# Optimization experiments

Measured on AMD Instinct MI355X. Metric: run time of the kernel, lower is better.

The kernel has to match this reference:

```python
import jax, jax.numpy as jnp
import numpy as np

B, T, I, H, O = 8192, 128, 28, 200, 10


def setup_inputs() -> dict:
    key = jax.random.key(0)
    ks = jax.random.split(key, 7)
    s_ih = 1.0 / np.sqrt(H)
    return {
        "x": jax.random.normal(ks[0], (B, T, I), dtype=jnp.float32),
        "W_ih": jax.random.uniform(ks[1], (H, I), jnp.float32, -s_ih, s_ih),
        "W_hh": jax.random.uniform(ks[2], (H, H), jnp.float32, -s_ih, s_ih),
        "b_ih": jax.random.uniform(ks[3], (H,), jnp.float32, -s_ih, s_ih),
        "b_hh": jax.random.uniform(ks[4], (H,), jnp.float32, -s_ih, s_ih),
        "W_fc": jax.random.uniform(ks[5], (O, H), jnp.float32, -s_ih, s_ih),
        "b_fc": jax.random.uniform(ks[6], (O,), jnp.float32, -s_ih, s_ih),
    }


def reference(x, W_ih, W_hh, b_ih, b_hh, W_fc, b_fc):
    # Precompute input projections for all timesteps in one GEMM: [B,T,H]
    xp = jnp.einsum("bti,hi->bth", x, W_ih) + b_ih + b_hh
    h0 = jnp.zeros((x.shape[0], W_hh.shape[0]), dtype=x.dtype)

    def step(h, xp_t):
        # h_t = relu(x_t W_ih^T + b_ih + h_{t-1} W_hh^T + b_hh)
        h = jax.nn.relu(xp_t + h @ W_hh.T)
        return h, None

    # scan over time: xp transposed to [T,B,H]
    h_last, _ = jax.lax.scan(step, h0, jnp.swapaxes(xp, 0, 1))
    # out[:, -1, :] then fc1
    return h_last @ W_fc.T + b_fc
```

## Files before the change

### kernel.cpp

```cpp
#include <hip/hip_runtime.h>

typedef float  f4v __attribute__((ext_vector_type(4)));
typedef float  f2v __attribute__((ext_vector_type(2)));
typedef short  s8v __attribute__((ext_vector_type(8)));

#define TT  128
#define II  28
#define HH  200
#define BB  16
#define NT  256
#define SH  264
#define KHX 208
#define SF  212

__device__ __forceinline__ short f2bf(float f) {
    union { float f; unsigned u; } a; a.f = f;
    unsigned r = a.u + 0x7FFFu + ((a.u >> 16) & 1u);
    return (short)(r >> 16);
}

__global__ __launch_bounds__(NT, 2)
void rnn_mfma(const float* __restrict__ x,
              const float* __restrict__ W_ih,
              const float* __restrict__ W_hh,
              const float* __restrict__ b_ih,
              const float* __restrict__ b_hh,
              const float* __restrict__ W_fc,
              const float* __restrict__ b_fc,
              float* __restrict__ out)
{
    __shared__ short Hs[BB][SH];
    __shared__ float Hf[BB][SF];
    __shared__ float bsum[208];

    const int tid  = threadIdx.x;
    const int lane = tid & 63;
    const int q    = lane >> 4;
    const int lr   = lane & 15;
    const int wave = tid >> 6;
    const int b0   = blockIdx.x * BB;

    const int first = (wave == 0) ? 0 : 1 + 3 * wave;
    const int cnt   = (wave == 0) ? 4 : 3;

    for (int i = tid; i < BB * SH / 2; i += NT) ((int*)Hs)[i] = 0;
    for (int j = tid; j < 208; j += NT) bsum[j] = (j < HH) ? b_ih[j] + b_hh[j] : 0.0f;

    s8v Af[4][8];
    #pragma unroll
    for (int u = 0; u < 4; ++u) {
        const int j = 16 * (first + u) + lr;
        #pragma unroll
        for (int kc = 0; kc < 8; ++kc) {
            const int k0 = 32 * kc + 8 * q;
            union { short s[8]; s8v v; } tv;
            #pragma unroll
            for (int i = 0; i < 8; ++i) {
                const int k = k0 + i;
                float w = 0.0f;
                if (u < cnt && j < HH) {
                    if (k < HH)                      w = W_hh[j * HH + k];
                    else if (k >= KHX && k < KHX+II) w = W_ih[j * II + (k - KHX)];
                }
                tv.s[i] = f2bf(w);
            }
            Af[u][kc] = tv.v;
        }
    }
    __syncthreads();

    f4v biasv[4];
    #pragma unroll
    for (int u = 0; u < 4; ++u) {
        const int jt = first + ((u < cnt) ? u : 0);
        biasv[u] = *(const f4v*)&bsum[16 * jt + 4 * q];
    }

    const int xr = tid / 14, xc = 2 * (tid % 14);
    f2v xcur = {0.f, 0.f}, xnxt = {0.f, 0.f};
    if (tid < 224) {
        f2v v0 = __builtin_nontemporal_load((const f2v*)&x[((b0 + xr) * TT + 0) * II + xc]);
        *(int*)&Hs[xr][KHX + xc] = (f2bf(v0.x) & 0xffff) | (f2bf(v0.y) << 16);
        xcur = __builtin_nontemporal_load((const f2v*)&x[((b0 + xr) * TT + 1) * II + xc]);
    }
    __syncthreads();

    for (int t = 0; t < TT; ++t) {
        if (tid < 224) {
            const int tn = (t + 2 < TT) ? t + 2 : TT - 1;
            xnxt = __builtin_nontemporal_load((const f2v*)&x[((b0 + xr) * TT + tn) * II + xc]);
        }

        f4v acc[4];
        #pragma unroll
        for (int u = 0; u < 4; ++u) acc[u] = biasv[u];

        #pragma unroll
        for (int kc = 0; kc < 8; ++kc) {
            const s8v bf = *(const s8v*)&Hs[lr][32 * kc + 8 * q];
            #pragma unroll
            for (int u = 0; u < 4; ++u)
                if (u < cnt)
                    acc[u] = __builtin_amdgcn_mfma_f32_16x16x32_bf16(Af[u][kc], bf, acc[u], 0, 0, 0);
        }
        __syncthreads();

        #pragma unroll
        for (int u = 0; u < 4; ++u) {
            if (u < cnt) {
                const int jt = first + u;
                const f4v a = acc[u];
                const float r0 = fmaxf(a.x, 0.f), r1 = fmaxf(a.y, 0.f);
                const float r2 = fmaxf(a.z, 0.f), r3 = fmaxf(a.w, 0.f);
                short4 hv;
                hv.x = f2bf(r0); hv.y = f2bf(r1); hv.z = f2bf(r2); hv.w = f2bf(r3);
                *(short4*)&Hs[lr][16 * jt + 4 * q] = hv;
                if (t == TT - 1) {
                    f4v rf = {r0, r1, r2, r3};
                    *(f4v*)&Hf[lr][16 * jt + 4 * q] = rf;
                }
            }
        }
        if (t < TT - 1 && tid < 224)
            *(int*)&Hs[xr][KHX + xc] = (f2bf(xcur.x) & 0xffff) | (f2bf(xcur.y) << 16);
        xcur = xnxt;
        __syncthreads();
    }

    if (tid < BB * 10) {
        const int o = tid >> 4, r = tid & 15;
        float s = b_fc[o];
        for (int k = 0; k < HH; ++k)
            s = fmaf(Hf[r][k], W_fc[o * HH + k], s);
        __builtin_nontemporal_store(s, &out[(b0 + r) * 10 + o]);
    }
}

extern "C" void kernel_launch(void* const* d_in, const int* in_sizes, int n_in,
                              void* d_out, int out_size, void* d_ws, size_t ws_size,
                              hipStream_t stream) {
    const float* x    = (const float*)d_in[0];
    const float* W_ih = (const float*)d_in[1];
    const float* W_hh = (const float*)d_in[2];
    const float* b_ih = (const float*)d_in[3];
    const float* b_hh = (const float*)d_in[4];
    const float* W_fc = (const float*)d_in[5];
    const float* b_fc = (const float*)d_in[6];
    float* out = (float*)d_out;

    rnn_mfma<<<dim3(8192 / BB), dim3(NT), 0, stream>>>(
        x, W_ih, W_hh, b_ih, b_hh, W_fc, b_fc, out);
}
```

Baseline: 322.6 us.

## Double-buffer hidden state and feed x directly as MFMA B operand

The hidden state in LDS becomes a ping-pong pair of buffers, which removes one of the two barriers per timestep. The input x_t is loaded straight into registers in MFMA B-fragment layout and used as the last K-chunk, rather than being staged through shared memory. Bias is read directly into registers without a shared-memory staging array. In exchange, each lane issues more global loads of x, unrolls the loop by two, and uses extra LDS for the second buffer.

New measurement: 318.5 us. Within noise of the previous version (-1.3%).

```diff
diff --git a/kernel.cpp b/kernel.cpp
--- a/kernel.cpp
+++ b/kernel.cpp
@@ -1,17 +1,16 @@
 #include <hip/hip_runtime.h>
 
-typedef float  f4v __attribute__((ext_vector_type(4)));
-typedef float  f2v __attribute__((ext_vector_type(2)));
-typedef short  s8v __attribute__((ext_vector_type(8)));
+typedef float f4v __attribute__((ext_vector_type(4)));
+typedef short s8v __attribute__((ext_vector_type(8)));
 
-#define TT  128
-#define II  28
-#define HH  200
-#define BB  16
-#define NT  256
-#define SH  264
-#define KHX 208
-#define SF  212
+#define TT 128
+#define II 28
+#define HH 200
+#define BB 16
+#define NT 256
+#define SH 232
+#define KX 224
+#define SF 212
 
 __device__ __forceinline__ short f2bf(float f) {
     union { float f; unsigned u; } a; a.f = f;
@@ -20,18 +19,17 @@
 }
 
 __global__ __launch_bounds__(NT, 2)
-void rnn_mfma(const float* __restrict__ x,
-              const float* __restrict__ W_ih,
-              const float* __restrict__ W_hh,
-              const float* __restrict__ b_ih,
-              const float* __restrict__ b_hh,
-              const float* __restrict__ W_fc,
-              const float* __restrict__ b_fc,
-              float* __restrict__ out)
+void rnn_mfma2(const float* __restrict__ x,
+               const float* __restrict__ W_ih,
+               const float* __restrict__ W_hh,
+               const float* __restrict__ b_ih,
+               const float* __restrict__ b_hh,
+               const float* __restrict__ W_fc,
+               const float* __restrict__ b_fc,
+               float* __restrict__ out)
 {
-    __shared__ short Hs[BB][SH];
-    __shared__ float Hf[BB][SF];
-    __shared__ float bsum[208];
+    __shared__ __align__(16) short Hs[2][BB][SH];
+    __shared__ __align__(16) float Hf[BB][SF];
 
     const int tid  = threadIdx.x;
     const int lane = tid & 63;
@@ -43,8 +41,7 @@
     const int first = (wave == 0) ? 0 : 1 + 3 * wave;
     const int cnt   = (wave == 0) ? 4 : 3;
 
-    for (int i = tid; i < BB * SH / 2; i += NT) ((int*)Hs)[i] = 0;
-    for (int j = tid; j < 208; j += NT) bsum[j] = (j < HH) ? b_ih[j] + b_hh[j] : 0.0f;
+    for (int i = tid; i < 2 * BB * SH / 2; i += NT) ((int*)Hs)[i] = 0;
 
     s8v Af[4][8];
     #pragma unroll
@@ -59,36 +56,45 @@
                 const int k = k0 + i;
                 float w = 0.0f;
                 if (u < cnt && j < HH) {
-                    if (k < HH)                      w = W_hh[j * HH + k];
-                    else if (k >= KHX && k < KHX+II) w = W_ih[j * II + (k - KHX)];
+                    if (k < HH)                     w = W_hh[j * HH + k];
+                    else if (k >= KX && k < KX+II)  w = W_ih[j * II + (k - KX)];
                 }
                 tv.s[i] = f2bf(w);
             }
             Af[u][kc] = tv.v;
         }
     }
-    __syncthreads();
 
     f4v biasv[4];
     #pragma unroll
     for (int u = 0; u < 4; ++u) {
-        const int jt = first + ((u < cnt) ? u : 0);
-        biasv[u] = *(const f4v*)&bsum[16 * jt + 4 * q];
+        const int jt = first + u;
+        f4v bv = {0.f, 0.f, 0.f, 0.f};
+        #pragma unroll
+        for (int i = 0; i < 4; ++i) {
+            const int j = 16 * jt + 4 * q + i;
+            if (u < cnt && j < HH) bv[i] = b_ih[j] + b_hh[j];
+        }
+        biasv[u] = bv;
     }
 
-    const int xr = tid / 14, xc = 2 * (tid % 14);
-    f2v xcur = {0.f, 0.f}, xnxt = {0.f, 0.f};
-    if (tid < 224) {
-        f2v v0 = __builtin_nontemporal_load((const f2v*)&x[((b0 + xr) * TT + 0) * II + xc]);
-        *(int*)&Hs[xr][KHX + xc] = (f2bf(v0.x) & 0xffff) | (f2bf(v0.y) << 16);
-        xcur = __builtin_nontemporal_load((const f2v*)&x[((b0 + xr) * TT + 1) * II + xc]);
-    }
+    const float* xp = x + (long)(b0 + lr) * TT * II + 8 * q;
+    f4v xa0 = {0,0,0,0}, xb0 = {0,0,0,0}, xa1 = {0,0,0,0}, xb1 = {0,0,0,0};
+    xa0 = *(const f4v*)(xp);
+    if (q != 3) xb0 = *(const f4v*)(xp + 4);
+    xa1 = *(const f4v*)(xp + II);
+    if (q != 3) xb1 = *(const f4v*)(xp + II + 4);
+
     __syncthreads();
 
-    for (int t = 0; t < TT; ++t) {
-        if (tid < 224) {
+    auto step = [&](int t, int pb, f4v& xa, f4v& xb) {
+        union { short s[8]; s8v v; } xf;
+        #pragma unroll
+        for (int i = 0; i < 4; ++i) { xf.s[i] = f2bf(xa[i]); xf.s[4+i] = f2bf(xb[i]); }
+        {
             const int tn = (t + 2 < TT) ? t + 2 : TT - 1;
-            xnxt = __builtin_nontemporal_load((const f2v*)&x[((b0 + xr) * TT + tn) * II + xc]);
+            xa = *(const f4v*)(xp + tn * II);
+            if (q != 3) xb = *(const f4v*)(xp + tn * II + 4);
         }
 
         f4v acc[4];
@@ -96,14 +102,17 @@
         for (int u = 0; u < 4; ++u) acc[u] = biasv[u];
 
         #pragma unroll
-        for (int kc = 0; kc < 8; ++kc) {
-            const s8v bf = *(const s8v*)&Hs[lr][32 * kc + 8 * q];
+        for (int kc = 0; kc < 7; ++kc) {
+            const s8v bf = *(const s8v*)&Hs[pb][lr][32 * kc + 8 * q];
             #pragma unroll
             for (int u = 0; u < 4; ++u)
                 if (u < cnt)
                     acc[u] = __builtin_amdgcn_mfma_f32_16x16x32_bf16(Af[u][kc], bf, acc[u], 0, 0, 0);
         }
-        __syncthreads();
+        #pragma unroll
+        for (int u = 0; u < 4; ++u)
+            if (u < cnt)
+                acc[u] = __builtin_amdgcn_mfma_f32_16x16x32_bf16(Af[u][7], xf.v, acc[u], 0, 0, 0);
 
         #pragma unroll
         for (int u = 0; u < 4; ++u) {
@@ -114,17 +123,19 @@
                 const float r2 = fmaxf(a.z, 0.f), r3 = fmaxf(a.w, 0.f);
                 short4 hv;
                 hv.x = f2bf(r0); hv.y = f2bf(r1); hv.z = f2bf(r2); hv.w = f2bf(r3);
-                *(short4*)&Hs[lr][16 * jt + 4 * q] = hv;
+                *(short4*)&Hs[pb ^ 1][lr][16 * jt + 4 * q] = hv;
                 if (t == TT - 1) {
                     f4v rf = {r0, r1, r2, r3};
                     *(f4v*)&Hf[lr][16 * jt + 4 * q] = rf;
                 }
             }
         }
-        if (t < TT - 1 && tid < 224)
-            *(int*)&Hs[xr][KHX + xc] = (f2bf(xcur.x) & 0xffff) | (f2bf(xcur.y) << 16);
-        xcur = xnxt;
         __syncthreads();
+    };
+
+    for (int tb = 0; tb < TT; tb += 2) {
+        step(tb,     0, xa0, xb0);
+        step(tb + 1, 1, xa1, xb1);
     }
 
     if (tid < BB * 10) {
@@ -148,6 +159,6 @@
     const float* b_fc = (const float*)d_in[6];
     float* out = (float*)d_out;
 
-    rnn_mfma<<<dim3(8192 / BB), dim3(NT), 0, stream>>>(
+    rnn_mfma2<<<dim3(8192 / BB), dim3(NT), 0, stream>>>(
         x, W_ih, W_hh, b_ih, b_hh, W_fc, b_fc, out);
 }
```
